# Optimization experiments

Measured on AMD Instinct MI355X. Metric: run time of the kernel, lower is better.

## Reference

```python
import jax, jax.numpy as jnp
import numpy as np

NUM_MODELS = 64
IN_F, HID, OUT_F = 6, 64, 3
LAYERS = 5
LN_EPS = 1e-5


def _mm_linear(x, W, B, idx):
    # W: [M, out, in], B: [M, out], x: [N, in], idx: [N]
    return jnp.einsum('nof,nf->no', W[idx], x) + B[idx]


def _mm_layernorm(x, g, b, idx):
    mu = jnp.mean(x, axis=-1, keepdims=True)
    var = jnp.mean((x - mu) ** 2, axis=-1, keepdims=True)
    xn = (x - mu) * jax.lax.rsqrt(var + LN_EPS)
    return xn * g[idx] + b[idx]


def setup_inputs() -> dict:
    key = jax.random.key(0)
    ks = jax.random.split(key, 16)
    N = 262144
    sqrt_k = float(np.sqrt(1.0 / NUM_MODELS))
    u = lambda k, shape: jax.random.uniform(k, shape, jnp.float32, -sqrt_k, sqrt_k)
    inp = {
        'x': jax.random.normal(ks[0], (N, IN_F), jnp.float32),
        'indices': jax.random.randint(ks[1], (N,), 0, NUM_MODELS),
        'W0': u(ks[2], (NUM_MODELS, HID, IN_F)), 'B0': u(ks[3], (NUM_MODELS, HID)),
        'G0': jnp.ones((NUM_MODELS, HID), jnp.float32), 'H0': jnp.zeros((NUM_MODELS, HID), jnp.float32),
        'W1': u(ks[4], (NUM_MODELS, HID, HID)), 'B1': u(ks[5], (NUM_MODELS, HID)),
        'G1': jnp.ones((NUM_MODELS, HID), jnp.float32), 'H1': jnp.zeros((NUM_MODELS, HID), jnp.float32),
        'W2': u(ks[6], (NUM_MODELS, HID, HID)), 'B2': u(ks[7], (NUM_MODELS, HID)),
        'G2': jnp.ones((NUM_MODELS, HID), jnp.float32), 'H2': jnp.zeros((NUM_MODELS, HID), jnp.float32),
        'W3': u(ks[8], (NUM_MODELS, HID, HID)), 'B3': u(ks[9], (NUM_MODELS, HID)),
        'G3': jnp.ones((NUM_MODELS, HID), jnp.float32), 'H3': jnp.zeros((NUM_MODELS, HID), jnp.float32),
        'W4': u(ks[10], (NUM_MODELS, OUT_F, HID)), 'B4': u(ks[11], (NUM_MODELS, OUT_F)),
    }
    return inp


def reference(x, indices, W0, B0, G0, H0, W1, B1, G1, H1, W2, B2, G2, H2, W3, B3, G3, H3, W4, B4):
    # forward_through_layers with use_layernorm=True, layers=5:
    Ws = [(W0, B0, G0, H0), (W1, B1, G1, H1), (W2, B2, G2, H2), (W3, B3, G3, H3)]
    h = x
    for W, B, G, Hb in Ws:
        h = _mm_linear(h, W, B, indices)
        h = _mm_layernorm(h, G, Hb, indices)
        h = jax.nn.relu(h)
    return _mm_linear(h, W4, B4, indices)  # [N, 3]
```

## Files before the change

kernel.cpp:

```cpp
#include <hip/hip_runtime.h>


#define NM    64
#define HIDD  64
#define INF   6
#define OUTF  3
#define CAP   4864
#define CSTRIDE 32
#define O_CURSORS 0
#define O_ORDER   2048
#define IWS_INTS  (O_ORDER + NM * CAP)

#define CONST_B   30720
#define NCONSTF   784
#define IMG_BYTES 33856

typedef _Float16 v8h __attribute__((ext_vector_type(8)));
typedef _Float16 v4h __attribute__((ext_vector_type(4)));
typedef float    v4f __attribute__((ext_vector_type(4)));

__global__ __launch_bounds__(256, 4) void bucket_prep_kernel(
    const int* __restrict__ idx, int n,
    const float* __restrict__ W0, const float* __restrict__ W1,
    const float* __restrict__ W2, const float* __restrict__ W3,
    const float* __restrict__ W4,
    const float* __restrict__ B0, const float* __restrict__ G0, const float* __restrict__ H0,
    const float* __restrict__ B1, const float* __restrict__ G1, const float* __restrict__ H1,
    const float* __restrict__ B2, const float* __restrict__ G2, const float* __restrict__ H2,
    const float* __restrict__ B3, const float* __restrict__ G3, const float* __restrict__ H3,
    const float* __restrict__ B4,
    int* __restrict__ iws, unsigned char* __restrict__ imgbase) {
    __shared__ int lcnt[NM];
    __shared__ int lbase[NM];
    const int b = blockIdx.x, t = threadIdx.x;
    const int m = b >> 3, sub = b & 7;
    _Float16* img = (_Float16*)(imgbase + (size_t)m * IMG_BYTES);
    float* cst = (float*)(imgbase + (size_t)m * IMG_BYTES + CONST_B);

    for (int s = sub * 256 + t; s < 1920; s += 2048) {
        int f = s >> 6, l = s & 63;
        int c = l & 15, q = l >> 4;
        float vals[8];
        if (f < 4) {
            const float* wr = W0 + m * 384 + (f * 16 + c) * 6;
#pragma unroll
            for (int j = 0; j < 8; j++) {
                int k = q * 8 + j;
                vals[j] = (k < INF) ? wr[k] : 0.0f;
            }
        } else if (f < 28) {
            int ll = (f - 4) >> 3, fb = (f - 4) & 7;
            int mt = fb >> 1, kh = fb & 1;
            const float* W = (ll == 0) ? W1 : (ll == 1) ? W2 : W3;
            const float* wr = W + m * 4096 + (mt * 16 + c) * 64 + kh * 32 + q * 8;
#pragma unroll
            for (int j = 0; j < 8; j++) vals[j] = wr[j];
        } else {
            int kh = f - 28;
            const float* wr = W4 + m * 192 + c * 64 + kh * 32 + q * 8;
#pragma unroll
            for (int j = 0; j < 8; j++) vals[j] = (c < OUTF) ? wr[j] : 0.0f;
        }
        v8h o;
#pragma unroll
        for (int j = 0; j < 8; j++) o[j] = (_Float16)vals[j];
        *(v8h*)(img + s * 8) = o;
    }
    {
        const float* lsrc[12] = {B0, G0, H0, B1, G1, H1, B2, G2, H2, B3, G3, H3};
        for (int e = sub * 256 + t; e < NCONSTF; e += 2048) {
            float v = 0.0f;
            if (e < 768) {
                int l = e / 192, r = e - l * 192;
                v = lsrc[l * 3 + (r >> 6)][m * 64 + (r & 63)];
            } else if (e < 771) {
                v = B4[m * 3 + (e - 768)];
            }
            cst[e] = v;
        }
    }

    if (t < NM) lcnt[t] = 0;
    __syncthreads();
    const int per = (n + gridDim.x - 1) / gridDim.x;
    const int beg = b * per, end = min(n, beg + per);
    int sidq[4], mmq[4], rrq[4];
    int qn = 0;
    for (int i = beg + t; i < end; i += 256) {
        sidq[qn] = i;
        mmq[qn] = idx[i];
        rrq[qn] = atomicAdd(&lcnt[mmq[qn]], 1);
        qn++;
    }
    __syncthreads();
    if (t < NM) lbase[t] = atomicAdd(&iws[O_CURSORS + t * CSTRIDE], lcnt[t]);
    __syncthreads();
    for (int j = 0; j < qn; j++)
        iws[O_ORDER + mmq[j] * CAP + lbase[mmq[j]] + rrq[j]] = sidq[j];
}

__device__ __forceinline__ void layer_epilogue(v4f D[4], const v4f gg[4], const v4f hh[4],
                                               _Float16* __restrict__ st) {
    float S = 0.0f, Q2 = 0.0f;
#pragma unroll
    for (int mt = 0; mt < 4; mt++)
#pragma unroll
        for (int r = 0; r < 4; r++) {
            float v = D[mt][r];
            S += v;
            Q2 = fmaf(v, v, Q2);
        }
    S += __shfl_xor(S, 16, 64);
    S += __shfl_xor(S, 32, 64);
    Q2 += __shfl_xor(Q2, 16, 64);
    Q2 += __shfl_xor(Q2, 32, 64);
    float mu = S * (1.0f / 64.0f);
    float var = Q2 * (1.0f / 64.0f) - mu * mu;
    float rs = rsqrtf(var + 1e-5f);
#pragma unroll
    for (int mt = 0; mt < 4; mt++) {
        v4h o;
#pragma unroll
        for (int r = 0; r < 4; r++) {
            float a = gg[mt][r] * rs;
            float bb = fmaf(-mu, a, hh[mt][r]);
            o[r] = (_Float16)fmaxf(fmaf(D[mt][r], a, bb), 0.0f);
        }
        *(v4h*)(st + mt * 16) = o;
    }
}

__global__ __launch_bounds__(256, 3) void mlp_kernel(
    const float* __restrict__ x,
    const int* __restrict__ iws,
    const unsigned char* __restrict__ imgbase,
    float* __restrict__ out) {
    __shared__ __align__(16) _Float16 s_H[4 * 64 * 72];

    const int m = blockIdx.y;
    const int cnt = iws[O_CURSORS + m * CSTRIDE];
    const int beg = m * CAP, end = beg + cnt;
    const int base = beg + blockIdx.x * 256;
    if (base >= end) return;

    const int t = threadIdx.x, w = t >> 6, lane = t & 63;
    const int c = lane & 15, q = lane >> 4;
    const int wbase = base + w * 64;
    if (wbase >= end) return;

    const _Float16* img = (const _Float16*)(imgbase + (size_t)m * IMG_BYTES);
    const float* cf = (const float*)(imgbase + (size_t)m * IMG_BYTES + CONST_B);
    _Float16* Hw = s_H + w * (64 * 72);
    const int* order = iws + O_ORDER;

    int sid[4];
#pragma unroll
    for (int ti = 0; ti < 4; ti++) {
        int p = wbase + ti * 16 + c;
        sid[ti] = order[p < end ? p : end - 1];
    }

    {
        v8h A[4];
#pragma unroll
        for (int mt = 0; mt < 4; mt++)
            A[mt] = *(const v8h*)(img + mt * 512 + lane * 8);
        v4f bias[4], gg[4], hh[4];
#pragma unroll
        for (int mt = 0; mt < 4; mt++) {
            bias[mt] = *(const v4f*)(cf + mt * 16 + q * 4);
            gg[mt]   = *(const v4f*)(cf + 64 + mt * 16 + q * 4);
            hh[mt]   = *(const v4f*)(cf + 128 + mt * 16 + q * 4);
        }
#pragma unroll
        for (int ti = 0; ti < 4; ti++) {
            v8h bfr = {0, 0, 0, 0, 0, 0, 0, 0};
            if (q == 0) {
                const float* xp = x + (size_t)sid[ti] * 6;
                float2 a0 = *(const float2*)(xp);
                float2 a1 = *(const float2*)(xp + 2);
                float2 a2 = *(const float2*)(xp + 4);
                bfr[0] = (_Float16)a0.x; bfr[1] = (_Float16)a0.y;
                bfr[2] = (_Float16)a1.x; bfr[3] = (_Float16)a1.y;
                bfr[4] = (_Float16)a2.x; bfr[5] = (_Float16)a2.y;
            }
            v4f D[4];
#pragma unroll
            for (int mt = 0; mt < 4; mt++)
                D[mt] = __builtin_amdgcn_mfma_f32_16x16x32_f16(A[mt], bfr, bias[mt], 0, 0, 0);
            layer_epilogue(D, gg, hh, Hw + (ti * 16 + c) * 72 + q * 4);
        }
    }

#pragma unroll 1
    for (int l = 1; l <= 3; l++) {
        const _Float16* wp = img + 2048 + (l - 1) * 4096 + lane * 8;
        v8h A[4][2];
#pragma unroll
        for (int mt = 0; mt < 4; mt++)
#pragma unroll
            for (int kh = 0; kh < 2; kh++)
                A[mt][kh] = *(const v8h*)(wp + (mt * 2 + kh) * 512);
        const float* cb = cf + l * 192;
        v4f bias[4], gg[4], hh[4];
#pragma unroll
        for (int mt = 0; mt < 4; mt++) {
            bias[mt] = *(const v4f*)(cb + mt * 16 + q * 4);
            gg[mt]   = *(const v4f*)(cb + 64 + mt * 16 + q * 4);
            hh[mt]   = *(const v4f*)(cb + 128 + mt * 16 + q * 4);
        }
#pragma unroll
        for (int ti = 0; ti < 4; ti++) {
            const _Float16* hp = Hw + (ti * 16 + c) * 72;
            v8h b0 = *(const v8h*)(hp + q * 8);
            v8h b1 = *(const v8h*)(hp + 32 + q * 8);
            v4f D[4];
#pragma unroll
            for (int mt = 0; mt < 4; mt++) {
                D[mt] = __builtin_amdgcn_mfma_f32_16x16x32_f16(A[mt][0], b0, bias[mt], 0, 0, 0);
                D[mt] = __builtin_amdgcn_mfma_f32_16x16x32_f16(A[mt][1], b1, D[mt], 0, 0, 0);
            }
            layer_epilogue(D, gg, hh, Hw + (ti * 16 + c) * 72 + q * 4);
        }
    }

    {
        const _Float16* wp = img + 14336 + lane * 8;
        v8h A0 = *(const v8h*)(wp);
        v8h A1 = *(const v8h*)(wp + 512);
        v4f b4i = {cf[768], cf[769], cf[770], 0.0f};
#pragma unroll
        for (int ti = 0; ti < 4; ti++) {
            const _Float16* hp = Hw + (ti * 16 + c) * 72;
            v8h b0 = *(const v8h*)(hp + q * 8);
            v8h b1 = *(const v8h*)(hp + 32 + q * 8);
            v4f D = __builtin_amdgcn_mfma_f32_16x16x32_f16(A0, b0, b4i, 0, 0, 0);
            D = __builtin_amdgcn_mfma_f32_16x16x32_f16(A1, b1, D, 0, 0, 0);
            int p = wbase + ti * 16 + c;
            if (q == 0 && p < end) {
                float* op = out + (size_t)sid[ti] * 3;
                op[0] = D[0]; op[1] = D[1]; op[2] = D[2];
            }
        }
    }
}

extern "C" void kernel_launch(void* const* d_in, const int* in_sizes, int n_in,
                              void* d_out, int out_size, void* d_ws, size_t ws_size,
                              hipStream_t stream) {
    const float* x  = (const float*)d_in[0];
    const int*  idx = (const int*)d_in[1];
    const float* W0 = (const float*)d_in[2];
    const float* B0 = (const float*)d_in[3];
    const float* G0 = (const float*)d_in[4];
    const float* H0 = (const float*)d_in[5];
    const float* W1 = (const float*)d_in[6];
    const float* B1 = (const float*)d_in[7];
    const float* G1 = (const float*)d_in[8];
    const float* H1 = (const float*)d_in[9];
    const float* W2 = (const float*)d_in[10];
    const float* B2 = (const float*)d_in[11];
    const float* G2 = (const float*)d_in[12];
    const float* H2 = (const float*)d_in[13];
    const float* W3 = (const float*)d_in[14];
    const float* B3 = (const float*)d_in[15];
    const float* G3 = (const float*)d_in[16];
    const float* H3 = (const float*)d_in[17];
    const float* W4 = (const float*)d_in[18];
    const float* B4 = (const float*)d_in[19];
    float* out = (float*)d_out;

    int n = in_sizes[1];
    int* iws = (int*)d_ws;
    unsigned char* imgbase = (unsigned char*)d_ws + (size_t)IWS_INTS * 4;

    hipMemsetAsync(d_ws, 0, NM * CSTRIDE * sizeof(int), stream);
    bucket_prep_kernel<<<dim3(512), 256, 0, stream>>>(
        idx, n, W0, W1, W2, W3, W4,
        B0, G0, H0, B1, G1, H1, B2, G2, H2, B3, G3, H3, B4, iws, imgbase);
    mlp_kernel<<<dim3(19, NM), 256, 0, stream>>>(x, iws, imgbase, out);
}
```

Measured before the change: 136.6 us.

## Drop fp16 weight-image prep; load fp32 weights directly in MLP kernel

Removes the weight/constant repacking from the bucketing kernel, which now only sorts sample indices, and halves its grid. The MLP kernel loads fp32 weights from the original tensors and converts them to fp16 fragments in registers. LayerNorm gamma/beta are loaded inside the epilogue instead of held in registers, and occupancy hints go up. The serial prep write and reread are gone, but every block now does more global loads and conversions for weights.

After: 159.7 us. 1.17x slower.

```diff
diff --git a/kernel.cpp b/kernel.cpp
--- a/kernel.cpp
+++ b/kernel.cpp
@@ -6,80 +6,19 @@
 #define INF   6
 #define OUTF  3
 #define CAP   4864
-#define CSTRIDE 32
+#define CSTRIDE   32
 #define O_CURSORS 0
 #define O_ORDER   2048
-#define IWS_INTS  (O_ORDER + NM * CAP)
-
-#define CONST_B   30720
-#define NCONSTF   784
-#define IMG_BYTES 33856
+#define HST   72
 
 typedef _Float16 v8h __attribute__((ext_vector_type(8)));
 typedef _Float16 v4h __attribute__((ext_vector_type(4)));
 typedef float    v4f __attribute__((ext_vector_type(4)));
 
-__global__ __launch_bounds__(256, 4) void bucket_prep_kernel(
-    const int* __restrict__ idx, int n,
-    const float* __restrict__ W0, const float* __restrict__ W1,
-    const float* __restrict__ W2, const float* __restrict__ W3,
-    const float* __restrict__ W4,
-    const float* __restrict__ B0, const float* __restrict__ G0, const float* __restrict__ H0,
-    const float* __restrict__ B1, const float* __restrict__ G1, const float* __restrict__ H1,
-    const float* __restrict__ B2, const float* __restrict__ G2, const float* __restrict__ H2,
-    const float* __restrict__ B3, const float* __restrict__ G3, const float* __restrict__ H3,
-    const float* __restrict__ B4,
-    int* __restrict__ iws, unsigned char* __restrict__ imgbase) {
-    __shared__ int lcnt[NM];
-    __shared__ int lbase[NM];
+__global__ __launch_bounds__(256, 8) void bucket_kernel(
+    const int* __restrict__ idx, int n, int* __restrict__ iws) {
+    __shared__ int lcnt[NM], lbase[NM];
     const int b = blockIdx.x, t = threadIdx.x;
-    const int m = b >> 3, sub = b & 7;
-    _Float16* img = (_Float16*)(imgbase + (size_t)m * IMG_BYTES);
-    float* cst = (float*)(imgbase + (size_t)m * IMG_BYTES + CONST_B);
-
-    for (int s = sub * 256 + t; s < 1920; s += 2048) {
-        int f = s >> 6, l = s & 63;
-        int c = l & 15, q = l >> 4;
-        float vals[8];
-        if (f < 4) {
-            const float* wr = W0 + m * 384 + (f * 16 + c) * 6;
-#pragma unroll
-            for (int j = 0; j < 8; j++) {
-                int k = q * 8 + j;
-                vals[j] = (k < INF) ? wr[k] : 0.0f;
-            }
-        } else if (f < 28) {
-            int ll = (f - 4) >> 3, fb = (f - 4) & 7;
-            int mt = fb >> 1, kh = fb & 1;
-            const float* W = (ll == 0) ? W1 : (ll == 1) ? W2 : W3;
-            const float* wr = W + m * 4096 + (mt * 16 + c) * 64 + kh * 32 + q * 8;
-#pragma unroll
-            for (int j = 0; j < 8; j++) vals[j] = wr[j];
-        } else {
-            int kh = f - 28;
-            const float* wr = W4 + m * 192 + c * 64 + kh * 32 + q * 8;
-#pragma unroll
-            for (int j = 0; j < 8; j++) vals[j] = (c < OUTF) ? wr[j] : 0.0f;
-        }
-        v8h o;
-#pragma unroll
-        for (int j = 0; j < 8; j++) o[j] = (_Float16)vals[j];
-        *(v8h*)(img + s * 8) = o;
-    }
-    {
-        const float* lsrc[12] = {B0, G0, H0, B1, G1, H1, B2, G2, H2, B3, G3, H3};
-        for (int e = sub * 256 + t; e < NCONSTF; e += 2048) {
-            float v = 0.0f;
-            if (e < 768) {
-                int l = e / 192, r = e - l * 192;
-                v = lsrc[l * 3 + (r >> 6)][m * 64 + (r & 63)];
-            } else if (e < 771) {
-                v = B4[m * 3 + (e - 768)];
-            }
-            cst[e] = v;
-        }
-    }
-
     if (t < NM) lcnt[t] = 0;
     __syncthreads();
     const int per = (n + gridDim.x - 1) / gridDim.x;
@@ -99,8 +38,19 @@
         iws[O_ORDER + mmq[j] * CAP + lbase[mmq[j]] + rrq[j]] = sidq[j];
 }
 
-__device__ __forceinline__ void layer_epilogue(v4f D[4], const v4f gg[4], const v4f hh[4],
-                                               _Float16* __restrict__ st) {
+__device__ __forceinline__ v8h cvt8(v4f a, v4f b) {
+    v8h r;
+    r[0] = (_Float16)a[0]; r[1] = (_Float16)a[1];
+    r[2] = (_Float16)a[2]; r[3] = (_Float16)a[3];
+    r[4] = (_Float16)b[0]; r[5] = (_Float16)b[1];
+    r[6] = (_Float16)b[2]; r[7] = (_Float16)b[3];
+    return r;
+}
+
+__device__ __forceinline__ void layer_epilogue(v4f D[4],
+                                               const float* __restrict__ gbase,
+                                               const float* __restrict__ hbase,
+                                               int q, _Float16* __restrict__ st) {
     float S = 0.0f, Q2 = 0.0f;
 #pragma unroll
     for (int mt = 0; mt < 4; mt++)
@@ -119,23 +69,32 @@
     float rs = rsqrtf(var + 1e-5f);
 #pragma unroll
     for (int mt = 0; mt < 4; mt++) {
+        v4f g = *(const v4f*)(gbase + mt * 16 + q * 4);
+        v4f h = *(const v4f*)(hbase + mt * 16 + q * 4);
         v4h o;
 #pragma unroll
         for (int r = 0; r < 4; r++) {
-            float a = gg[mt][r] * rs;
-            float bb = fmaf(-mu, a, hh[mt][r]);
+            float a = g[r] * rs;
+            float bb = fmaf(-mu, a, h[r]);
             o[r] = (_Float16)fmaxf(fmaf(D[mt][r], a, bb), 0.0f);
         }
         *(v4h*)(st + mt * 16) = o;
     }
 }
 
-__global__ __launch_bounds__(256, 3) void mlp_kernel(
-    const float* __restrict__ x,
-    const int* __restrict__ iws,
-    const unsigned char* __restrict__ imgbase,
+__global__ __launch_bounds__(256, 4) void mlp_kernel(
+    const float* __restrict__ x, const int* __restrict__ iws,
+    const float* __restrict__ W0, const float* __restrict__ B0,
+    const float* __restrict__ G0, const float* __restrict__ H0,
+    const float* __restrict__ W1, const float* __restrict__ B1,
+    const float* __restrict__ G1, const float* __restrict__ H1,
+    const float* __restrict__ W2, const float* __restrict__ B2,
+    const float* __restrict__ G2, const float* __restrict__ H2,
+    const float* __restrict__ W3, const float* __restrict__ B3,
+    const float* __restrict__ G3, const float* __restrict__ H3,
+    const float* __restrict__ W4, const float* __restrict__ B4,
     float* __restrict__ out) {
-    __shared__ __align__(16) _Float16 s_H[4 * 64 * 72];
+    __shared__ __align__(16) _Float16 s_H[4 * 64 * HST];
 
     const int m = blockIdx.y;
     const int cnt = iws[O_CURSORS + m * CSTRIDE];
@@ -148,9 +107,7 @@
     const int wbase = base + w * 64;
     if (wbase >= end) return;
 
-    const _Float16* img = (const _Float16*)(imgbase + (size_t)m * IMG_BYTES);
-    const float* cf = (const float*)(imgbase + (size_t)m * IMG_BYTES + CONST_B);
-    _Float16* Hw = s_H + w * (64 * 72);
+    _Float16* Hw = s_H + w * (64 * HST);
     const int* order = iws + O_ORDER;
 
     int sid[4];
@@ -161,20 +118,26 @@
     }
 
     {
-        v8h A[4];
+        v8h A[4] = {};
+        if (q == 0) {
+#pragma unroll
+            for (int mt = 0; mt < 4; mt++) {
+                const float* wp = W0 + m * 384 + (mt * 16 + c) * 6;
+                float2 a0 = *(const float2*)(wp);
+                float2 a1 = *(const float2*)(wp + 2);
+                float2 a2 = *(const float2*)(wp + 4);
+                A[mt][0] = (_Float16)a0.x; A[mt][1] = (_Float16)a0.y;
+                A[mt][2] = (_Float16)a1.x; A[mt][3] = (_Float16)a1.y;
+                A[mt][4] = (_Float16)a2.x; A[mt][5] = (_Float16)a2.y;
+            }
+        }
+        v4f bias[4];
 #pragma unroll
         for (int mt = 0; mt < 4; mt++)
-            A[mt] = *(const v8h*)(img + mt * 512 + lane * 8);
-        v4f bias[4], gg[4], hh[4];
-#pragma unroll
-        for (int mt = 0; mt < 4; mt++) {
-            bias[mt] = *(const v4f*)(cf + mt * 16 + q * 4);
-            gg[mt]   = *(const v4f*)(cf + 64 + mt * 16 + q * 4);
-            hh[mt]   = *(const v4f*)(cf + 128 + mt * 16 + q * 4);
-        }
+            bias[mt] = *(const v4f*)(B0 + m * 64 + mt * 16 + q * 4);
 #pragma unroll
         for (int ti = 0; ti < 4; ti++) {
-            v8h bfr = {0, 0, 0, 0, 0, 0, 0, 0};
+            v8h bfr = {};
             if (q == 0) {
                 const float* xp = x + (size_t)sid[ti] * 6;
                 float2 a0 = *(const float2*)(xp);
@@ -188,30 +151,34 @@
 #pragma unroll
             for (int mt = 0; mt < 4; mt++)
                 D[mt] = __builtin_amdgcn_mfma_f32_16x16x32_f16(A[mt], bfr, bias[mt], 0, 0, 0);
-            layer_epilogue(D, gg, hh, Hw + (ti * 16 + c) * 72 + q * 4);
-        }
-    }
-
+            layer_epilogue(D, G0 + m * 64, H0 + m * 64, q,
+                           Hw + (ti * 16 + c) * HST + q * 4);
+        }
+    }
+
+    const float* Wl[3] = {W1, W2, W3};
+    const float* Bl[3] = {B1, B2, B3};
+    const float* Gl[3] = {G1, G2, G3};
+    const float* Hl[3] = {H1, H2, H3};
 #pragma unroll 1
-    for (int l = 1; l <= 3; l++) {
-        const _Float16* wp = img + 2048 + (l - 1) * 4096 + lane * 8;
+    for (int l = 0; l < 3; l++) {
+        const float* wp = Wl[l] + m * 4096 + c * 64 + q * 8;
         v8h A[4][2];
 #pragma unroll
         for (int mt = 0; mt < 4; mt++)
 #pragma unroll
-            for (int kh = 0; kh < 2; kh++)
-                A[mt][kh] = *(const v8h*)(wp + (mt * 2 + kh) * 512);
-        const float* cb = cf + l * 192;
-        v4f bias[4], gg[4], hh[4];
-#pragma unroll
-        for (int mt = 0; mt < 4; mt++) {
-            bias[mt] = *(const v4f*)(cb + mt * 16 + q * 4);
-            gg[mt]   = *(const v4f*)(cb + 64 + mt * 16 + q * 4);
-            hh[mt]   = *(const v4f*)(cb + 128 + mt * 16 + q * 4);
-        }
+            for (int kh = 0; kh < 2; kh++) {
+                v4f u0 = *(const v4f*)(wp + mt * 1024 + kh * 32);
+                v4f u1 = *(const v4f*)(wp + mt * 1024 + kh * 32 + 4);
+                A[mt][kh] = cvt8(u0, u1);
+            }
+        v4f bias[4];
+#pragma unroll
+        for (int mt = 0; mt < 4; mt++)
+            bias[mt] = *(const v4f*)(Bl[l] + m * 64 + mt * 16 + q * 4);
 #pragma unroll
         for (int ti = 0; ti < 4; ti++) {
-            const _Float16* hp = Hw + (ti * 16 + c) * 72;
+            const _Float16* hp = Hw + (ti * 16 + c) * HST;
             v8h b0 = *(const v8h*)(hp + q * 8);
             v8h b1 = *(const v8h*)(hp + 32 + q * 8);
             v4f D[4];
@@ -220,22 +187,31 @@
                 D[mt] = __builtin_amdgcn_mfma_f32_16x16x32_f16(A[mt][0], b0, bias[mt], 0, 0, 0);
                 D[mt] = __builtin_amdgcn_mfma_f32_16x16x32_f16(A[mt][1], b1, D[mt], 0, 0, 0);
             }
-            layer_epilogue(D, gg, hh, Hw + (ti * 16 + c) * 72 + q * 4);
+            layer_epilogue(D, Gl[l] + m * 64, Hl[l] + m * 64, q,
+                           Hw + (ti * 16 + c) * HST + q * 4);
         }
     }
 
     {
-        const _Float16* wp = img + 14336 + lane * 8;
-        v8h A0 = *(const v8h*)(wp);
-        v8h A1 = *(const v8h*)(wp + 512);
-        v4f b4i = {cf[768], cf[769], cf[770], 0.0f};
+        v8h A4[2] = {};
+        if (c < OUTF) {
+            const float* wp = W4 + m * 192 + c * 64 + q * 8;
+            A4[0] = cvt8(*(const v4f*)(wp), *(const v4f*)(wp + 4));
+            A4[1] = cvt8(*(const v4f*)(wp + 32), *(const v4f*)(wp + 36));
+        }
+        v4f b4i = {0.0f, 0.0f, 0.0f, 0.0f};
+        if (q == 0) {
+            b4i[0] = B4[m * 3 + 0];
+            b4i[1] = B4[m * 3 + 1];
+            b4i[2] = B4[m * 3 + 2];
+        }
 #pragma unroll
         for (int ti = 0; ti < 4; ti++) {
-            const _Float16* hp = Hw + (ti * 16 + c) * 72;
+            const _Float16* hp = Hw + (ti * 16 + c) * HST;
             v8h b0 = *(const v8h*)(hp + q * 8);
             v8h b1 = *(const v8h*)(hp + 32 + q * 8);
-            v4f D = __builtin_amdgcn_mfma_f32_16x16x32_f16(A0, b0, b4i, 0, 0, 0);
-            D = __builtin_amdgcn_mfma_f32_16x16x32_f16(A1, b1, D, 0, 0, 0);
+            v4f D = __builtin_amdgcn_mfma_f32_16x16x32_f16(A4[0], b0, b4i, 0, 0, 0);
+            D = __builtin_amdgcn_mfma_f32_16x16x32_f16(A4[1], b1, D, 0, 0, 0);
             int p = wbase + ti * 16 + c;
             if (q == 0 && p < end) {
                 float* op = out + (size_t)sid[ti] * 3;
@@ -272,11 +248,10 @@
 
     int n = in_sizes[1];
     int* iws = (int*)d_ws;
-    unsigned char* imgbase = (unsigned char*)d_ws + (size_t)IWS_INTS * 4;
 
     hipMemsetAsync(d_ws, 0, NM * CSTRIDE * sizeof(int), stream);
-    bucket_prep_kernel<<<dim3(512), 256, 0, stream>>>(
-        idx, n, W0, W1, W2, W3, W4,
-        B0, G0, H0, B1, G1, H1, B2, G2, H2, B3, G3, H3, B4, iws, imgbase);
-    mlp_kernel<<<dim3(19, NM), 256, 0, stream>>>(x, iws, imgbase, out);
-}
+    bucket_kernel<<<dim3(256), 256, 0, stream>>>(idx, n, iws);
+    mlp_kernel<<<dim3(19, NM), 256, 0, stream>>>(
+        x, iws, W0, B0, G0, H0, W1, B1, G1, H1, W2, B2, G2, H2,
+        W3, B3, G3, H3, W4, B4, out);
+}
```

## Replace atomic bucketing with histogram-scan-scatter and pre-sorted fp16 inputs

Applied to the files above, without the earlier changes.

Splits the prep into a per-block histogram kernel, a serial scan kernel, and a scatter kernel that writes both the order array and a bucket-contiguous fp16 copy of x. The MLP kernel then reads inputs contiguously instead of gathering scattered fp32 rows, drops the memset, and raises its occupancy hint from 3 to 4. The cost is two extra kernel launches, a serial 256-step scan on a single wave, and an extra pass over idx and x.

After: 146.9 us. +7.5%, slower.

```diff
diff --git a/kernel.cpp b/kernel.cpp
--- a/kernel.cpp
+++ b/kernel.cpp
@@ -6,20 +6,25 @@
 #define INF   6
 #define OUTF  3
 #define CAP   4864
-#define CSTRIDE 32
-#define O_CURSORS 0
-#define O_ORDER   2048
-#define IWS_INTS  (O_ORDER + NM * CAP)
+#define NBLK  256
+
+#define O_COUNTS 0
+#define O_HIST   64
+#define O_BASE   (O_HIST + NBLK * 64)
+#define O_ORDER  (O_BASE + NBLK * 64)
+#define IWS_INTS (O_ORDER + NM * CAP)
 
 #define CONST_B   30720
 #define NCONSTF   784
 #define IMG_BYTES 33856
 
+#define HST 72
+
 typedef _Float16 v8h __attribute__((ext_vector_type(8)));
 typedef _Float16 v4h __attribute__((ext_vector_type(4)));
 typedef float    v4f __attribute__((ext_vector_type(4)));
 
-__global__ __launch_bounds__(256, 4) void bucket_prep_kernel(
+__global__ __launch_bounds__(256, 4) void hist_img_kernel(
     const int* __restrict__ idx, int n,
     const float* __restrict__ W0, const float* __restrict__ W1,
     const float* __restrict__ W2, const float* __restrict__ W3,
@@ -30,14 +35,13 @@
     const float* __restrict__ B3, const float* __restrict__ G3, const float* __restrict__ H3,
     const float* __restrict__ B4,
     int* __restrict__ iws, unsigned char* __restrict__ imgbase) {
-    __shared__ int lcnt[NM];
-    __shared__ int lbase[NM];
+    __shared__ int lc[NM];
     const int b = blockIdx.x, t = threadIdx.x;
-    const int m = b >> 3, sub = b & 7;
+    const int m = b >> 2, sub = b & 3;
+
     _Float16* img = (_Float16*)(imgbase + (size_t)m * IMG_BYTES);
     float* cst = (float*)(imgbase + (size_t)m * IMG_BYTES + CONST_B);
-
-    for (int s = sub * 256 + t; s < 1920; s += 2048) {
+    for (int s = sub * 256 + t; s < 1920; s += 1024) {
         int f = s >> 6, l = s & 63;
         int c = l & 15, q = l >> 4;
         float vals[8];
@@ -64,11 +68,12 @@
         v8h o;
 #pragma unroll
         for (int j = 0; j < 8; j++) o[j] = (_Float16)vals[j];
-        *(v8h*)(img + s * 8) = o;
+        *(v8h*)(img + (size_t)s * 8) = o;
     }
     {
         const float* lsrc[12] = {B0, G0, H0, B1, G1, H1, B2, G2, H2, B3, G3, H3};
-        for (int e = sub * 256 + t; e < NCONSTF; e += 2048) {
+        int e = sub * 256 + t;
+        if (e < NCONSTF) {
             float v = 0.0f;
             if (e < 768) {
                 int l = e / 192, r = e - l * 192;
@@ -80,9 +85,34 @@
         }
     }
 
+    if (t < NM) lc[t] = 0;
+    __syncthreads();
+    const int per = (n + NBLK - 1) / NBLK;
+    const int beg = b * per, end = min(n, beg + per);
+    for (int i = beg + t; i < end; i += 256) atomicAdd(&lc[idx[i]], 1);
+    __syncthreads();
+    if (t < NM) iws[O_HIST + b * NM + t] = lc[t];
+}
+
+__global__ void scan_kernel(int* __restrict__ iws) {
+    const int m = threadIdx.x;
+    int run = 0;
+    for (int b = 0; b < NBLK; b++) {
+        int v = iws[O_HIST + b * NM + m];
+        iws[O_BASE + b * NM + m] = run;
+        run += v;
+    }
+    iws[O_COUNTS + m] = run;
+}
+
+__global__ __launch_bounds__(256, 4) void scatter_kernel(
+    const int* __restrict__ idx, const float* __restrict__ x, int n,
+    int* __restrict__ iws, _Float16* __restrict__ xs) {
+    __shared__ int lcnt[NM], lbase[NM];
+    const int b = blockIdx.x, t = threadIdx.x;
     if (t < NM) lcnt[t] = 0;
     __syncthreads();
-    const int per = (n + gridDim.x - 1) / gridDim.x;
+    const int per = (n + NBLK - 1) / NBLK;
     const int beg = b * per, end = min(n, beg + per);
     int sidq[4], mmq[4], rrq[4];
     int qn = 0;
@@ -93,10 +123,21 @@
         qn++;
     }
     __syncthreads();
-    if (t < NM) lbase[t] = atomicAdd(&iws[O_CURSORS + t * CSTRIDE], lcnt[t]);
-    __syncthreads();
-    for (int j = 0; j < qn; j++)
-        iws[O_ORDER + mmq[j] * CAP + lbase[mmq[j]] + rrq[j]] = sidq[j];
+    if (t < NM) lbase[t] = iws[O_BASE + b * NM + t];
+    __syncthreads();
+    for (int j = 0; j < qn; j++) {
+        int slot = mmq[j] * CAP + lbase[mmq[j]] + rrq[j];
+        iws[O_ORDER + slot] = sidq[j];
+        const float* xp = x + (size_t)sidq[j] * 6;
+        float2 a0 = *(const float2*)(xp);
+        float2 a1 = *(const float2*)(xp + 2);
+        float2 a2 = *(const float2*)(xp + 4);
+        v8h o = {};
+        o[0] = (_Float16)a0.x; o[1] = (_Float16)a0.y;
+        o[2] = (_Float16)a1.x; o[3] = (_Float16)a1.y;
+        o[4] = (_Float16)a2.x; o[5] = (_Float16)a2.y;
+        *(v8h*)(xs + (size_t)slot * 8) = o;
+    }
 }
 
 __device__ __forceinline__ void layer_epilogue(v4f D[4], const v4f gg[4], const v4f hh[4],
@@ -130,15 +171,13 @@
     }
 }
 
-__global__ __launch_bounds__(256, 3) void mlp_kernel(
-    const float* __restrict__ x,
-    const int* __restrict__ iws,
-    const unsigned char* __restrict__ imgbase,
-    float* __restrict__ out) {
-    __shared__ __align__(16) _Float16 s_H[4 * 64 * 72];
+__global__ __launch_bounds__(256, 4) void mlp_kernel(
+    const int* __restrict__ iws, const _Float16* __restrict__ xs,
+    const unsigned char* __restrict__ imgbase, float* __restrict__ out) {
+    __shared__ __align__(16) _Float16 s_H[4 * 64 * HST];
 
     const int m = blockIdx.y;
-    const int cnt = iws[O_CURSORS + m * CSTRIDE];
+    const int cnt = iws[O_COUNTS + m];
     const int beg = m * CAP, end = beg + cnt;
     const int base = beg + blockIdx.x * 256;
     if (base >= end) return;
@@ -150,14 +189,15 @@
 
     const _Float16* img = (const _Float16*)(imgbase + (size_t)m * IMG_BYTES);
     const float* cf = (const float*)(imgbase + (size_t)m * IMG_BYTES + CONST_B);
-    _Float16* Hw = s_H + w * (64 * 72);
+    _Float16* Hw = s_H + w * (64 * HST);
     const int* order = iws + O_ORDER;
 
-    int sid[4];
+    int sid[4], sp[4];
 #pragma unroll
     for (int ti = 0; ti < 4; ti++) {
         int p = wbase + ti * 16 + c;
-        sid[ti] = order[p < end ? p : end - 1];
+        sp[ti] = p < end ? p : end - 1;
+        sid[ti] = order[sp[ti]];
     }
 
     {
@@ -174,21 +214,13 @@
         }
 #pragma unroll
         for (int ti = 0; ti < 4; ti++) {
-            v8h bfr = {0, 0, 0, 0, 0, 0, 0, 0};
-            if (q == 0) {
-                const float* xp = x + (size_t)sid[ti] * 6;
-                float2 a0 = *(const float2*)(xp);
-                float2 a1 = *(const float2*)(xp + 2);
-                float2 a2 = *(const float2*)(xp + 4);
-                bfr[0] = (_Float16)a0.x; bfr[1] = (_Float16)a0.y;
-                bfr[2] = (_Float16)a1.x; bfr[3] = (_Float16)a1.y;
-                bfr[4] = (_Float16)a2.x; bfr[5] = (_Float16)a2.y;
-            }
+            v8h bfr = {};
+            if (q == 0) bfr = *(const v8h*)(xs + (size_t)sp[ti] * 8);
             v4f D[4];
 #pragma unroll
             for (int mt = 0; mt < 4; mt++)
                 D[mt] = __builtin_amdgcn_mfma_f32_16x16x32_f16(A[mt], bfr, bias[mt], 0, 0, 0);
-            layer_epilogue(D, gg, hh, Hw + (ti * 16 + c) * 72 + q * 4);
+            layer_epilogue(D, gg, hh, Hw + (ti * 16 + c) * HST + q * 4);
         }
     }
 
@@ -211,7 +243,7 @@
         }
 #pragma unroll
         for (int ti = 0; ti < 4; ti++) {
-            const _Float16* hp = Hw + (ti * 16 + c) * 72;
+            const _Float16* hp = Hw + (ti * 16 + c) * HST;
             v8h b0 = *(const v8h*)(hp + q * 8);
             v8h b1 = *(const v8h*)(hp + 32 + q * 8);
             v4f D[4];
@@ -220,7 +252,7 @@
                 D[mt] = __builtin_amdgcn_mfma_f32_16x16x32_f16(A[mt][0], b0, bias[mt], 0, 0, 0);
                 D[mt] = __builtin_amdgcn_mfma_f32_16x16x32_f16(A[mt][1], b1, D[mt], 0, 0, 0);
             }
-            layer_epilogue(D, gg, hh, Hw + (ti * 16 + c) * 72 + q * 4);
+            layer_epilogue(D, gg, hh, Hw + (ti * 16 + c) * HST + q * 4);
         }
     }
 
@@ -231,7 +263,7 @@
         v4f b4i = {cf[768], cf[769], cf[770], 0.0f};
 #pragma unroll
         for (int ti = 0; ti < 4; ti++) {
-            const _Float16* hp = Hw + (ti * 16 + c) * 72;
+            const _Float16* hp = Hw + (ti * 16 + c) * HST;
             v8h b0 = *(const v8h*)(hp + q * 8);
             v8h b1 = *(const v8h*)(hp + 32 + q * 8);
             v4f D = __builtin_amdgcn_mfma_f32_16x16x32_f16(A0, b0, b4i, 0, 0, 0);
@@ -272,11 +304,14 @@
 
     int n = in_sizes[1];
     int* iws = (int*)d_ws;
-    unsigned char* imgbase = (unsigned char*)d_ws + (size_t)IWS_INTS * 4;
-
-    hipMemsetAsync(d_ws, 0, NM * CSTRIDE * sizeof(int), stream);
-    bucket_prep_kernel<<<dim3(512), 256, 0, stream>>>(
+    _Float16* xs = (_Float16*)((char*)d_ws + (size_t)IWS_INTS * 4);
+    unsigned char* imgbase =
+        (unsigned char*)d_ws + (size_t)IWS_INTS * 4 + (size_t)NM * CAP * 16;
+
+    hist_img_kernel<<<dim3(NBLK), 256, 0, stream>>>(
         idx, n, W0, W1, W2, W3, W4,
         B0, G0, H0, B1, G1, H1, B2, G2, H2, B3, G3, H3, B4, iws, imgbase);
-    mlp_kernel<<<dim3(19, NM), 256, 0, stream>>>(x, iws, imgbase, out);
-}
+    scan_kernel<<<1, 64, 0, stream>>>(iws);
+    scatter_kernel<<<dim3(NBLK), 256, 0, stream>>>(idx, x, n, iws, xs);
+    mlp_kernel<<<dim3(19, NM), 256, 0, stream>>>(iws, xs, imgbase, out);
+}
```
